# Optimization experiments

Hardware: AMD Instinct MI355X
Metric: run time of the kernel (lower is better)

## Reference

```python
import jax, jax.numpy as jnp
import numpy as np

B, H, T, D = 2, 8, 2048, 64
STATE = H * D  # 512

def setup_inputs() -> dict:
    key = jax.random.key(0)
    kq, kk, kv, kw, kl = jax.random.split(key, 5)
    q = jax.random.normal(kq, (B * H, T, D), jnp.float32)
    k = jax.random.normal(kk, (B * H, T, D), jnp.float32)
    v = jax.random.normal(kv, (B * H, T, D), jnp.float32)
    # causal position mask: True = masked (future positions)
    position_mask = jnp.triu(jnp.ones((T, T), dtype=bool), 1)
    # per-batch source lengths in [T//2, T]; True = padding (masked)
    lengths = jax.random.randint(kl, (B,), T // 2, T + 1)
    src_length_mask = jnp.arange(T)[None, :] >= lengths[:, None]
    W_merge = jax.random.normal(kw, (STATE, STATE), jnp.float32) / np.sqrt(STATE)
    return {"q": q, "k": k, "v": v, "position_mask": position_mask,
            "src_length_mask": src_length_mask, "W_merge": W_merge}

def reference(q, k, v, position_mask, src_length_mask, W_merge):
    bb, n_dest, d = q.shape              # bb = B*H
    n_batch = src_length_mask.shape[0]
    n_heads = bb // n_batch
    scale = 1.0 / np.sqrt(d)
    # [bb, T_dest, T_src] full score matrix (as in the torch bmm)
    logits = jnp.einsum('btd,bsd->bts', q, k) * scale
    logits = logits.reshape(n_batch, n_heads, n_dest, -1)
    logits = jnp.where(position_mask[None, None], -jnp.inf, logits)
    logits = jnp.where(src_length_mask[:, None, None, :], -jnp.inf, logits)
    scores = jax.nn.softmax(logits, axis=-1).reshape(bb, n_dest, -1)
    # dropout p=0 (eval) -> identity
    out = jnp.einsum('bts,bsd->btd', scores, v)
    out = out.reshape(n_batch, n_heads, n_dest, d).transpose(0, 2, 1, 3)
    out = out.reshape(n_batch, n_dest, n_heads * d)
    return out @ W_merge.T  # bias-free Linear merge
```

## Files before the change

### kernel.cpp

```cpp
#include <hip/hip_runtime.h>

#define TT 2048
#define DD 64
#define NSTATE 512

typedef __attribute__((ext_vector_type(8))) short short8;
typedef __attribute__((ext_vector_type(4))) short short4v;
typedef __attribute__((ext_vector_type(4))) float f4;

__device__ __forceinline__ short f2bf(float x) {
  union { float f; unsigned u; } c; c.f = x;
  unsigned r = (c.u + 0x7FFFu + ((c.u >> 16) & 1u)) >> 16;
  return (short)r;
}

__device__ __forceinline__ bool mask_at(const void* p, bool u8, int idx) {
  return u8 ? (((const unsigned char*)p)[idx] != 0)
            : (((const int*)p)[idx] != 0);
}

__device__ __forceinline__ void gld16(const void* g, void* l) {
  __builtin_amdgcn_global_load_lds(
      (const __attribute__((address_space(1))) void*)g,
      (__attribute__((address_space(3))) void*)l, 16, 0, 0);
}

__global__ __launch_bounds__(256)
void prep_kernel(const float* __restrict__ k, const float* __restrict__ v,
                 const float* __restrict__ W, const void* __restrict__ posmask,
                 const void* __restrict__ srcmask,
                 unsigned short* __restrict__ Wb, unsigned short* __restrict__ Kimg,
                 unsigned short* __restrict__ VTimg, int* __restrict__ lenbuf) {
  const int bidx = blockIdx.x;
  const int tid = threadIdx.x;
  if (bidx < 512) {
    const int bh = bidx >> 5, tile = bidx & 31;
    const float* kp = k + (bh * TT + tile * 64) * DD;
    unsigned short* dst = Kimg + (bh * 32 + tile) * 4096;
#pragma unroll
    for (int t2 = 0; t2 < 2; ++t2) {
      int j = tid + t2 * 256;
      int c8 = j >> 6, r6 = j & 63;
      int kb = c8 >> 1, cc = c8 & 1, qd = r6 >> 4, klo = r6 & 15;
      int key = kb * 16 + klo, dg = cc * 4 + qd;
      f4 a0 = *(const f4*)(kp + key * DD + dg * 8);
      f4 a1 = *(const f4*)(kp + key * DD + dg * 8 + 4);
      short8 o;
      o[0]=f2bf(a0[0]); o[1]=f2bf(a0[1]); o[2]=f2bf(a0[2]); o[3]=f2bf(a0[3]);
      o[4]=f2bf(a1[0]); o[5]=f2bf(a1[1]); o[6]=f2bf(a1[2]); o[7]=f2bf(a1[3]);
      *(short8*)(dst + j * 8) = o;
    }
    __shared__ float Vt[64][65];
    const float* vp = v + (bh * TT + tile * 64) * DD;
    {
      int key = tid >> 2, c0 = (tid & 3) * 16;
#pragma unroll
      for (int i = 0; i < 4; ++i) {
        f4 x = *(const f4*)(vp + key * DD + c0 + i * 4);
        Vt[key][c0 + i * 4 + 0] = x[0];
        Vt[key][c0 + i * 4 + 1] = x[1];
        Vt[key][c0 + i * 4 + 2] = x[2];
        Vt[key][c0 + i * 4 + 3] = x[3];
      }
    }
    __syncthreads();
    unsigned short* vd = VTimg + (bh * 32 + tile) * 4096;
#pragma unroll
    for (int t2 = 0; t2 < 2; ++t2) {
      int j = tid + t2 * 256;
      int fs = j >> 5;
      int db = fs >> 2, sb = fs & 3;
      int jj = j & 31;
      short8 o;
#pragma unroll
      for (int ii = 0; ii < 8; ++ii) {
        int l = jj * 2 + (ii >> 2), r = ii & 3;
        int s = sb * 16 + (l >> 4) * 4 + r;
        int d = db * 16 + (l & 15);
        o[ii] = f2bf(Vt[s][d]);
      }
      *(short8*)(vd + j * 8) = o;
    }
  } else if (bidx < 768) {
    int i = ((bidx - 512) * 256 + tid) * 4;
    f4 x = *(const f4*)(W + i);
    short4v o;
    o[0]=f2bf(x[0]); o[1]=f2bf(x[1]); o[2]=f2bf(x[2]); o[3]=f2bf(x[3]);
    *(short4v*)(Wb + i) = o;
  } else {
    const int wv = tid >> 6, lane = tid & 63;
    if (wv < 2) {
      const bool u8 = (((const unsigned char*)posmask)[1] != 0);
      int pos = 1024 + lane * 16;
      bool m1 = mask_at(srcmask, u8, wv * TT + pos);
      unsigned long long bal = __ballot(m1);
      int cur = bal ? (1024 + (__ffsll((unsigned long long)bal) - 1) * 16) : 2048;
      int prev = cur - 16;
      bool m2 = false;
      if (lane < 16) {
        int pos2 = prev + 1 + lane;
        m2 = (pos2 < TT) ? mask_at(srcmask, u8, wv * TT + pos2) : true;
      }
      unsigned long long bal2 = __ballot(m2);
      int len = prev + 1 + (__ffsll((unsigned long long)bal2) - 1);
      if (lane == 0) lenbuf[wv] = len;
    }
  }
}

__global__ __launch_bounds__(256)
void attn_kernel(const float* __restrict__ q, const unsigned short* __restrict__ Kimg,
                 const unsigned short* __restrict__ VTimg,
                 const int* __restrict__ lenbuf, unsigned short* __restrict__ merged) {
  const int i = blockIdx.x;
  const int bh = ((i & 7) << 1) | ((i >> 3) & 1);
  const int tr = i >> 4;
  const int tile = (tr < 16) ? tr : 47 - tr;
  const int b = bh >> 3, h = bh & 7;
  const int tid = threadIdx.x;
  const int w = tid >> 6, lane = tid & 63;
  const int lane_lo = lane & 15, quad = lane >> 4;
  const int q0 = tile * 64 + w * 16;
  const int len = lenbuf[b];
  const int n_st = min(tile + 1, (len + 63) >> 6);

  __shared__ __attribute__((aligned(16))) unsigned short Klds[2][4096];
  __shared__ __attribute__((aligned(16))) unsigned short Vlds[2][4096];

  short8 qf[2];
  {
    const float* qrow = q + ((bh * TT) + q0 + lane_lo) * DD;
#pragma unroll
    for (int c = 0; c < 2; ++c) {
      int d0 = c * 32 + quad * 8;
      f4 a0 = *(const f4*)(qrow + d0);
      f4 a1 = *(const f4*)(qrow + d0 + 4);
      short8 t;
      t[0]=f2bf(a0[0]*0.125f); t[1]=f2bf(a0[1]*0.125f);
      t[2]=f2bf(a0[2]*0.125f); t[3]=f2bf(a0[3]*0.125f);
      t[4]=f2bf(a1[0]*0.125f); t[5]=f2bf(a1[1]*0.125f);
      t[6]=f2bf(a1[2]*0.125f); t[7]=f2bf(a1[3]*0.125f);
      qf[c] = t;
    }
  }

  float l_lane = 0.f;
  f4 O[4];
#pragma unroll
  for (int d = 0; d < 4; ++d) O[d] = (f4){0.f, 0.f, 0.f, 0.f};

  const char* kbase = (const char*)Kimg + (size_t)bh * 262144;
  const char* vbase = (const char*)VTimg + (size_t)bh * 262144;

  auto stage = [&](int st, int bufi) {
    const char* ks = kbase + st * 8192 + w * 2048 + lane * 16;
    char* kl = (char*)&Klds[bufi][0] + w * 2048 + lane * 16;
    gld16(ks, kl); gld16(ks + 1024, kl + 1024);
    const char* vs = vbase + st * 8192 + w * 2048 + lane * 16;
    char* vl = (char*)&Vlds[bufi][0] + w * 2048 + lane * 16;
    gld16(vs, vl); gld16(vs + 1024, vl + 1024);
  };

  stage(0, 0);
  __syncthreads();

  for (int st = 0; st < n_st; ++st) {
    const int bufc = st & 1;
    if (st + 1 < n_st) stage(st + 1, bufc ^ 1);
    const unsigned short* Kl = Klds[bufc];
    const unsigned short* Vl = Vlds[bufc];
    const int s0 = st * 64;

    f4 ST[4];
    __builtin_amdgcn_s_setprio(1);
#pragma unroll
    for (int sb = 0; sb < 4; ++sb) {
      f4 acc = (f4){0.f, 0.f, 0.f, 0.f};
#pragma unroll
      for (int c = 0; c < 2; ++c) {
        short8 kf = *(const short8*)&Kl[((sb * 2 + c) * 64 + lane) * 8];
        acc = __builtin_amdgcn_mfma_f32_16x16x32_bf16(kf, qf[c], acc, 0, 0, 0);
      }
      ST[sb] = acc;
    }
    __builtin_amdgcn_s_setprio(0);

    const bool edge = (st == tile) || (s0 + 64 > len);
    const int tq = q0 + lane_lo;
    short4v pf[4];
#pragma unroll
    for (int sb = 0; sb < 4; ++sb)
#pragma unroll
      for (int r = 0; r < 4; ++r) {
        float p = __expf(ST[sb][r]);
        if (edge) {
          int s = s0 + sb * 16 + quad * 4 + r;
          if (s > tq || s >= len) p = 0.f;
        }
        l_lane += p;
        pf[sb][r] = f2bf(p);
      }

    __builtin_amdgcn_s_setprio(1);
#pragma unroll
    for (int db = 0; db < 4; ++db) {
      f4 acc = O[db];
#pragma unroll
      for (int sb = 0; sb < 4; ++sb) {
        short4v vf = *(const short4v*)&Vl[(db * 4 + sb) * 256 + lane * 4];
        acc = __builtin_amdgcn_mfma_f32_16x16x16bf16_1k(pf[sb], vf, acc, 0, 0, 0);
      }
      O[db] = acc;
    }
    __builtin_amdgcn_s_setprio(0);
    __syncthreads();
  }

  l_lane += __shfl_xor(l_lane, 16);
  l_lane += __shfl_xor(l_lane, 32);
  float inv = 1.0f / l_lane;
  float invr[4];
#pragma unroll
  for (int r = 0; r < 4; ++r) invr[r] = __shfl(inv, quad * 4 + r);
#pragma unroll
  for (int db = 0; db < 4; ++db)
#pragma unroll
    for (int r = 0; r < 4; ++r) {
      int t = q0 + quad * 4 + r;
      merged[((b * TT) + t) * NSTATE + h * DD + db * 16 + lane_lo] =
          (unsigned short)f2bf(O[db][r] * invr[r]);
    }
}

__global__ __launch_bounds__(256)
void merge_kernel(const unsigned short* __restrict__ A,
                  const unsigned short* __restrict__ Wb,
                  float* __restrict__ out) {
  __shared__ __attribute__((aligned(16))) unsigned short Wl[64 * 512];
  const int tid = threadIdx.x;
  const int n0 = blockIdx.x * 64, m0 = blockIdx.y * 64;
  {
    int row = tid >> 2, cb = (tid & 3) * 16;
    const unsigned short* src = Wb + (n0 + row) * NSTATE;
#pragma unroll
    for (int j = 0; j < 16; ++j) {
      int c = cb + j;
      int phys = c ^ (row & 7);
      *(short8*)&Wl[row * 512 + phys * 8] = *(const short8*)(src + c * 8);
    }
  }
  __syncthreads();

  const int w = tid >> 6, lane = tid & 63;
  const int lo16 = lane & 15, quad = lane >> 4;
  const int m = m0 + w * 16;
  f4 acc[4];
#pragma unroll
  for (int nf = 0; nf < 4; ++nf) acc[nf] = (f4){0.f, 0.f, 0.f, 0.f};
  const unsigned short* arow = A + (m + lo16) * NSTATE + quad * 8;
#pragma unroll 4
  for (int k0 = 0; k0 < NSTATE; k0 += 32) {
    short8 af = *(const short8*)(arow + k0);
#pragma unroll
    for (int nf = 0; nf < 4; ++nf) {
      int n = nf * 16 + lo16;
      int phys = ((k0 >> 3) + quad) ^ (n & 7);
      short8 bf = *(const short8*)&Wl[n * 512 + phys * 8];
      acc[nf] = __builtin_amdgcn_mfma_f32_16x16x32_bf16(af, bf, acc[nf], 0, 0, 0);
    }
  }
#pragma unroll
  for (int nf = 0; nf < 4; ++nf)
#pragma unroll
    for (int r = 0; r < 4; ++r)
      out[(m + quad * 4 + r) * NSTATE + n0 + nf * 16 + lo16] = acc[nf][r];
}

extern "C" void kernel_launch(void* const* d_in, const int* in_sizes, int n_in,
                              void* d_out, int out_size, void* d_ws, size_t ws_size,
                              hipStream_t stream) {
  (void)in_sizes; (void)n_in; (void)out_size; (void)ws_size;
  const float* q = (const float*)d_in[0];
  const float* k = (const float*)d_in[1];
  const float* v = (const float*)d_in[2];
  const void* posm = d_in[3];
  const void* srcm = d_in[4];
  const float* W = (const float*)d_in[5];
  float* out = (float*)d_out;

  unsigned short* merged = (unsigned short*)d_ws;
  unsigned short* Wb     = merged + 2097152;
  unsigned short* Kimg   = Wb + 262144;
  unsigned short* VTimg  = Kimg + 2097152;
  int* lenbuf = (int*)(VTimg + 2097152);

  prep_kernel<<<dim3(769), dim3(256), 0, stream>>>(k, v, W, posm, srcm,
                                                   Wb, Kimg, VTimg, lenbuf);
  attn_kernel<<<dim3(512), dim3(256), 0, stream>>>(q, Kimg, VTimg, lenbuf, merged);
  merge_kernel<<<dim3(8, 64), dim3(256), 0, stream>>>(merged, Wb, out);
}
```

Before: 131.5 us.

## Split attention KV range into chunks with a separate combine kernel

Long causal query tiles now have their KV loop split into chunks of eight stages, each chunk handled by its own block, so the grid grows from 512 to 1280 blocks with more even per-block work. Each chunk writes unnormalized fp32 partial outputs and row sums, and a new combine kernel adds them, normalizes, and writes the bf16 merged tensor. This addresses load imbalance and tail effects from the triangular causal workload. It adds an extra kernel launch and a large fp32 partial-output round trip through memory. Summing partials without rescaling assumes every chunk uses the same fixed softmax offset.

```diff
diff --git a/kernel.cpp b/kernel.cpp
--- a/kernel.cpp
+++ b/kernel.cpp
@@ -111,18 +111,27 @@
 __global__ __launch_bounds__(256)
 void attn_kernel(const float* __restrict__ q, const unsigned short* __restrict__ Kimg,
                  const unsigned short* __restrict__ VTimg,
-                 const int* __restrict__ lenbuf, unsigned short* __restrict__ merged) {
+                 const int* __restrict__ lenbuf, float* __restrict__ Opart,
+                 float* __restrict__ lpart) {
   const int i = blockIdx.x;
   const int bh = ((i & 7) << 1) | ((i >> 3) & 1);
-  const int tr = i >> 4;
-  const int tile = (tr < 16) ? tr : 47 - tr;
+  const int e = i >> 4;
+  int tile, c0;
+  if (e < 8)       { tile = e;                 c0 = 0; }
+  else if (e < 24) { tile = 8 + ((e - 8) >> 1);  c0 = (e - 8) & 1; }
+  else if (e < 48) { tile = 16 + (e - 24) / 3;   c0 = (e - 24) % 3; }
+  else             { tile = 24 + ((e - 48) >> 2); c0 = (e - 48) & 3; }
   const int b = bh >> 3, h = bh & 7;
+  const int len = lenbuf[b];
+  const int n_st = min(tile + 1, (len + 63) >> 6);
+  const int st_begin = c0 * 8;
+  const int st_end = min(st_begin + 8, n_st);
+  if (st_begin >= st_end) return;
+
   const int tid = threadIdx.x;
   const int w = tid >> 6, lane = tid & 63;
   const int lane_lo = lane & 15, quad = lane >> 4;
   const int q0 = tile * 64 + w * 16;
-  const int len = lenbuf[b];
-  const int n_st = min(tile + 1, (len + 63) >> 6);
 
   __shared__ __attribute__((aligned(16))) unsigned short Klds[2][4096];
   __shared__ __attribute__((aligned(16))) unsigned short Vlds[2][4096];
@@ -161,12 +170,12 @@
     gld16(vs, vl); gld16(vs + 1024, vl + 1024);
   };
 
-  stage(0, 0);
+  stage(st_begin, 0);
   __syncthreads();
 
-  for (int st = 0; st < n_st; ++st) {
-    const int bufc = st & 1;
-    if (st + 1 < n_st) stage(st + 1, bufc ^ 1);
+  for (int st = st_begin; st < st_end; ++st) {
+    const int bufc = (st - st_begin) & 1;
+    if (st + 1 < st_end) stage(st + 1, bufc ^ 1);
     const unsigned short* Kl = Klds[bufc];
     const unsigned short* Vl = Vlds[bufc];
     const int s0 = st * 64;
@@ -218,18 +227,42 @@
 
   l_lane += __shfl_xor(l_lane, 16);
   l_lane += __shfl_xor(l_lane, 32);
-  float inv = 1.0f / l_lane;
-  float invr[4];
-#pragma unroll
-  for (int r = 0; r < 4; ++r) invr[r] = __shfl(inv, quad * 4 + r);
+  if (quad == 0) lpart[(c0 * 16 + bh) * TT + q0 + lane_lo] = l_lane;
+  float* ob = Opart + (size_t)c0 * 4096 * NSTATE;
 #pragma unroll
   for (int db = 0; db < 4; ++db)
 #pragma unroll
     for (int r = 0; r < 4; ++r) {
       int t = q0 + quad * 4 + r;
-      merged[((b * TT) + t) * NSTATE + h * DD + db * 16 + lane_lo] =
-          (unsigned short)f2bf(O[db][r] * invr[r]);
-    }
+      ob[((b * TT) + t) * NSTATE + h * DD + db * 16 + lane_lo] = O[db][r];
+    }
+}
+
+__global__ __launch_bounds__(256)
+void combine_kernel(const float* __restrict__ Opart, const float* __restrict__ lpart,
+                    const int* __restrict__ lenbuf, unsigned short* __restrict__ merged) {
+  const int tid = threadIdx.x;
+  const int m = blockIdx.x * 2 + (tid >> 7);
+  const int col = (tid & 127) * 4;
+  const int b = m >> 11, t = m & 2047;
+  const int qt = t >> 6;
+  const int len = lenbuf[b];
+  const int nst = min(qt + 1, (len + 63) >> 6);
+  const int C = (nst + 7) >> 3;
+  const int h = col >> 6;
+  const int bh = b * 8 + h;
+  float l_tot = 0.f;
+  f4 osum = (f4){0.f, 0.f, 0.f, 0.f};
+  for (int c = 0; c < C; ++c) {
+    l_tot += lpart[(c * 16 + bh) * TT + t];
+    f4 o = *(const f4*)(Opart + ((size_t)c * 4096 + m) * NSTATE + col);
+    osum[0] += o[0]; osum[1] += o[1]; osum[2] += o[2]; osum[3] += o[3];
+  }
+  float inv = 1.0f / l_tot;
+  short4v r;
+  r[0] = f2bf(osum[0] * inv); r[1] = f2bf(osum[1] * inv);
+  r[2] = f2bf(osum[2] * inv); r[3] = f2bf(osum[3] * inv);
+  *(short4v*)(merged + (size_t)m * NSTATE + col) = r;
 }
 
 __global__ __launch_bounds__(256)
@@ -288,7 +321,9 @@
   const float* W = (const float*)d_in[5];
   float* out = (float*)d_out;
 
-  unsigned short* merged = (unsigned short*)d_ws;
+  float* Opart = (float*)d_ws;
+  float* lpart = Opart + 4 * 4096 * NSTATE;
+  unsigned short* merged = (unsigned short*)(lpart + 4 * 16 * TT);
   unsigned short* Wb     = merged + 2097152;
   unsigned short* Kimg   = Wb + 262144;
   unsigned short* VTimg  = Kimg + 2097152;
@@ -296,6 +331,8 @@
 
   prep_kernel<<<dim3(769), dim3(256), 0, stream>>>(k, v, W, posm, srcm,
                                                    Wb, Kimg, VTimg, lenbuf);
-  attn_kernel<<<dim3(512), dim3(256), 0, stream>>>(q, Kimg, VTimg, lenbuf, merged);
+  attn_kernel<<<dim3(1280), dim3(256), 0, stream>>>(q, Kimg, VTimg, lenbuf,
+                                                    Opart, lpart);
+  combine_kernel<<<dim3(2048), dim3(256), 0, stream>>>(Opart, lpart, lenbuf, merged);
   merge_kernel<<<dim3(8, 64), dim3(256), 0, stream>>>(merged, Wb, out);
 }
```

New measurement: 132.3 us. Within noise of the previous version (+0.6%).

## Split attention KV loop across two wave groups and enlarge merge tiles

Applied to the files above, without the earlier changes.

Each attention block now runs 8 waves in two groups. The groups process alternating KV tiles, each into its own double-buffered LDS region, and their partial O and row sums are combined through shared memory at the end. This is meant to double the waves working per query tile and cut the serial KV loop length, especially for long causal rows. The cost is twice the LDS per block plus a final reduction and barrier. The merge kernel also moves to 512 threads covering 128 rows per block, which halves how many times W is staged into LDS.

```diff
diff --git a/kernel.cpp b/kernel.cpp
--- a/kernel.cpp
+++ b/kernel.cpp
@@ -108,7 +108,7 @@
   }
 }
 
-__global__ __launch_bounds__(256)
+__global__ __launch_bounds__(512, 4)
 void attn_kernel(const float* __restrict__ q, const unsigned short* __restrict__ Kimg,
                  const unsigned short* __restrict__ VTimg,
                  const int* __restrict__ lenbuf, unsigned short* __restrict__ merged) {
@@ -119,13 +119,15 @@
   const int b = bh >> 3, h = bh & 7;
   const int tid = threadIdx.x;
   const int w = tid >> 6, lane = tid & 63;
+  const int g = w >> 2, wl = w & 3;
   const int lane_lo = lane & 15, quad = lane >> 4;
-  const int q0 = tile * 64 + w * 16;
+  const int q0 = tile * 64 + wl * 16;
   const int len = lenbuf[b];
   const int n_st = min(tile + 1, (len + 63) >> 6);
-
-  __shared__ __attribute__((aligned(16))) unsigned short Klds[2][4096];
-  __shared__ __attribute__((aligned(16))) unsigned short Vlds[2][4096];
+  const int trips = (n_st + 1) >> 1;
+
+  __shared__ __attribute__((aligned(16))) unsigned short Klds[2][2][4096];
+  __shared__ __attribute__((aligned(16))) unsigned short Vlds[2][2][4096];
 
   short8 qf[2];
   {
@@ -153,97 +155,121 @@
   const char* vbase = (const char*)VTimg + (size_t)bh * 262144;
 
   auto stage = [&](int st, int bufi) {
-    const char* ks = kbase + st * 8192 + w * 2048 + lane * 16;
-    char* kl = (char*)&Klds[bufi][0] + w * 2048 + lane * 16;
+    const char* ks = kbase + st * 8192 + wl * 2048 + lane * 16;
+    char* kl = (char*)&Klds[g][bufi][0] + wl * 2048 + lane * 16;
     gld16(ks, kl); gld16(ks + 1024, kl + 1024);
-    const char* vs = vbase + st * 8192 + w * 2048 + lane * 16;
-    char* vl = (char*)&Vlds[bufi][0] + w * 2048 + lane * 16;
+    const char* vs = vbase + st * 8192 + wl * 2048 + lane * 16;
+    char* vl = (char*)&Vlds[g][bufi][0] + wl * 2048 + lane * 16;
     gld16(vs, vl); gld16(vs + 1024, vl + 1024);
   };
 
-  stage(0, 0);
+  if (g < n_st) stage(g, 0);
   __syncthreads();
 
-  for (int st = 0; st < n_st; ++st) {
-    const int bufc = st & 1;
-    if (st + 1 < n_st) stage(st + 1, bufc ^ 1);
-    const unsigned short* Kl = Klds[bufc];
-    const unsigned short* Vl = Vlds[bufc];
-    const int s0 = st * 64;
-
-    f4 ST[4];
-    __builtin_amdgcn_s_setprio(1);
-#pragma unroll
-    for (int sb = 0; sb < 4; ++sb) {
-      f4 acc = (f4){0.f, 0.f, 0.f, 0.f};
-#pragma unroll
-      for (int c = 0; c < 2; ++c) {
-        short8 kf = *(const short8*)&Kl[((sb * 2 + c) * 64 + lane) * 8];
-        acc = __builtin_amdgcn_mfma_f32_16x16x32_bf16(kf, qf[c], acc, 0, 0, 0);
-      }
-      ST[sb] = acc;
-    }
-    __builtin_amdgcn_s_setprio(0);
-
-    const bool edge = (st == tile) || (s0 + 64 > len);
-    const int tq = q0 + lane_lo;
-    short4v pf[4];
-#pragma unroll
-    for (int sb = 0; sb < 4; ++sb)
-#pragma unroll
-      for (int r = 0; r < 4; ++r) {
-        float p = __expf(ST[sb][r]);
-        if (edge) {
-          int s = s0 + sb * 16 + quad * 4 + r;
-          if (s > tq || s >= len) p = 0.f;
+  for (int it = 0; it < trips; ++it) {
+    const int st = 2 * it + g;
+    const int bufc = it & 1;
+    const int st_next = st + 2;
+    if (st_next < n_st) stage(st_next, bufc ^ 1);
+    if (st < n_st) {
+      const unsigned short* Kl = &Klds[g][bufc][0];
+      const unsigned short* Vl = &Vlds[g][bufc][0];
+      const int s0 = st * 64;
+
+      f4 ST[4];
+      __builtin_amdgcn_s_setprio(1);
+#pragma unroll
+      for (int sb = 0; sb < 4; ++sb) {
+        f4 acc = (f4){0.f, 0.f, 0.f, 0.f};
+#pragma unroll
+        for (int c = 0; c < 2; ++c) {
+          short8 kf = *(const short8*)&Kl[((sb * 2 + c) * 64 + lane) * 8];
+          acc = __builtin_amdgcn_mfma_f32_16x16x32_bf16(kf, qf[c], acc, 0, 0, 0);
         }
-        l_lane += p;
-        pf[sb][r] = f2bf(p);
-      }
-
-    __builtin_amdgcn_s_setprio(1);
-#pragma unroll
-    for (int db = 0; db < 4; ++db) {
-      f4 acc = O[db];
-#pragma unroll
-      for (int sb = 0; sb < 4; ++sb) {
-        short4v vf = *(const short4v*)&Vl[(db * 4 + sb) * 256 + lane * 4];
-        acc = __builtin_amdgcn_mfma_f32_16x16x16bf16_1k(pf[sb], vf, acc, 0, 0, 0);
-      }
-      O[db] = acc;
-    }
-    __builtin_amdgcn_s_setprio(0);
+        ST[sb] = acc;
+      }
+      __builtin_amdgcn_s_setprio(0);
+
+      const bool edge = (st == tile) || (s0 + 64 > len);
+      const int tq = q0 + lane_lo;
+      short4v pf[4];
+#pragma unroll
+      for (int sb = 0; sb < 4; ++sb)
+#pragma unroll
+        for (int r = 0; r < 4; ++r) {
+          float p = __expf(ST[sb][r]);
+          if (edge) {
+            int s = s0 + sb * 16 + quad * 4 + r;
+            if (s > tq || s >= len) p = 0.f;
+          }
+          l_lane += p;
+          pf[sb][r] = f2bf(p);
+        }
+
+      __builtin_amdgcn_s_setprio(1);
+#pragma unroll
+      for (int db = 0; db < 4; ++db) {
+        f4 acc = O[db];
+#pragma unroll
+        for (int sb = 0; sb < 4; ++sb) {
+          short4v vf = *(const short4v*)&Vl[(db * 4 + sb) * 256 + lane * 4];
+          acc = __builtin_amdgcn_mfma_f32_16x16x16bf16_1k(pf[sb], vf, acc, 0, 0, 0);
+        }
+        O[db] = acc;
+      }
+      __builtin_amdgcn_s_setprio(0);
+    }
     __syncthreads();
   }
 
   l_lane += __shfl_xor(l_lane, 16);
   l_lane += __shfl_xor(l_lane, 32);
-  float inv = 1.0f / l_lane;
-  float invr[4];
-#pragma unroll
-  for (int r = 0; r < 4; ++r) invr[r] = __shfl(inv, quad * 4 + r);
-#pragma unroll
-  for (int db = 0; db < 4; ++db)
-#pragma unroll
-    for (int r = 0; r < 4; ++r) {
-      int t = q0 + quad * 4 + r;
-      merged[((b * TT) + t) * NSTATE + h * DD + db * 16 + lane_lo] =
-          (unsigned short)f2bf(O[db][r] * invr[r]);
-    }
-}
-
-__global__ __launch_bounds__(256)
+
+  float* Ored = (float*)&Klds[1][0][0];
+  float* lred = (float*)&Vlds[1][0][0];
+  if (g == 1) {
+    float* po = Ored + (wl * 64 + lane) * 16;
+#pragma unroll
+    for (int db = 0; db < 4; ++db) *(f4*)(po + db * 4) = O[db];
+    lred[wl * 64 + lane] = l_lane;
+  }
+  __syncthreads();
+  if (g == 0) {
+    const float* po = Ored + (wl * 64 + lane) * 16;
+#pragma unroll
+    for (int db = 0; db < 4; ++db) {
+      f4 o1 = *(const f4*)(po + db * 4);
+      O[db][0] += o1[0]; O[db][1] += o1[1];
+      O[db][2] += o1[2]; O[db][3] += o1[3];
+    }
+    l_lane += lred[wl * 64 + lane];
+    float inv = 1.0f / l_lane;
+    float invr[4];
+#pragma unroll
+    for (int r = 0; r < 4; ++r) invr[r] = __shfl(inv, quad * 4 + r);
+#pragma unroll
+    for (int db = 0; db < 4; ++db)
+#pragma unroll
+      for (int r = 0; r < 4; ++r) {
+        int t = q0 + quad * 4 + r;
+        merged[((b * TT) + t) * NSTATE + h * DD + db * 16 + lane_lo] =
+            (unsigned short)f2bf(O[db][r] * invr[r]);
+      }
+  }
+}
+
+__global__ __launch_bounds__(512)
 void merge_kernel(const unsigned short* __restrict__ A,
                   const unsigned short* __restrict__ Wb,
                   float* __restrict__ out) {
   __shared__ __attribute__((aligned(16))) unsigned short Wl[64 * 512];
   const int tid = threadIdx.x;
-  const int n0 = blockIdx.x * 64, m0 = blockIdx.y * 64;
+  const int n0 = blockIdx.x * 64, m0 = blockIdx.y * 128;
   {
-    int row = tid >> 2, cb = (tid & 3) * 16;
+    int row = tid >> 3, cb = (tid & 7) * 8;
     const unsigned short* src = Wb + (n0 + row) * NSTATE;
 #pragma unroll
-    for (int j = 0; j < 16; ++j) {
+    for (int j = 0; j < 8; ++j) {
       int c = cb + j;
       int phys = c ^ (row & 7);
       *(short8*)&Wl[row * 512 + phys * 8] = *(const short8*)(src + c * 8);
@@ -296,6 +322,6 @@
 
   prep_kernel<<<dim3(769), dim3(256), 0, stream>>>(k, v, W, posm, srcm,
                                                    Wb, Kimg, VTimg, lenbuf);
-  attn_kernel<<<dim3(512), dim3(256), 0, stream>>>(q, Kimg, VTimg, lenbuf, merged);
-  merge_kernel<<<dim3(8, 64), dim3(256), 0, stream>>>(merged, Wb, out);
-}
+  attn_kernel<<<dim3(512), dim3(512), 0, stream>>>(q, Kimg, VTimg, lenbuf, merged);
+  merge_kernel<<<dim3(8, 32), dim3(512), 0, stream>>>(merged, Wb, out);
+}
```

Result: faster. 122.2 us (-7.0%).
